# Kernel optimization log

Measured on AMD Instinct MI355X. Metric: run time of the kernel, lower is better.

Reference implementation:

```python
import jax, jax.numpy as jnp
import numpy as np

B, N, D = 32, 1024, 256
NHID = 512
NHID_HALF = NHID // 2
NCLASS = 2


def _xavier(key, shape):
    fan_in, fan_out = shape
    lim = float(np.sqrt(6.0 / (fan_in + fan_out)))
    return jax.random.uniform(key, shape, jnp.float32, -lim, lim)


def setup_inputs() -> dict:
    key = jax.random.key(0)
    ks = jax.random.split(key, 10)
    x = jax.random.normal(ks[0], (B, N, D), jnp.float32)
    adj = jax.random.uniform(ks[1], (B, N, N), jnp.float32)
    adj = adj / jnp.sum(adj, axis=-1, keepdims=True)  # row-normalized (mean aggregation)
    # GraphConv weights: shape (2*in_dim, out_dim) due to concat([x, agg(x)])
    W1 = _xavier(ks[2], (2 * D, NHID))
    b1 = jnp.zeros((NHID,), jnp.float32)
    W2 = _xavier(ks[3], (2 * NHID, NHID))
    b2 = jnp.zeros((NHID,), jnp.float32)
    W3 = _xavier(ks[4], (2 * NHID, NHID_HALF))
    b3 = jnp.zeros((NHID_HALF,), jnp.float32)
    W4 = _xavier(ks[5], (2 * NHID_HALF, NHID_HALF))
    b4 = jnp.zeros((NHID_HALF,), jnp.float32)
    # classifier: Linear(256,256) + PReLU(256) + Linear(256,2)
    cW1 = _xavier(ks[6], (NHID_HALF, NHID_HALF))
    cb1 = jnp.zeros((NHID_HALF,), jnp.float32)
    alpha = jnp.full((NHID_HALF,), 0.25, jnp.float32)
    cW2 = _xavier(ks[7], (NHID_HALF, NCLASS))
    cb2 = jnp.zeros((NCLASS,), jnp.float32)
    return {"x": x, "adj": adj, "W1": W1, "b1": b1, "W2": W2, "b2": b2,
            "W3": W3, "b3": b3, "W4": W4, "b4": b4,
            "cW1": cW1, "cb1": cb1, "alpha": alpha, "cW2": cW2, "cb2": cb2}


def _graphconv(x, adj, W, b):
    agg = jnp.einsum('bnm,bmd->bnd', adj, x)          # mean aggregation (adj row-normalized)
    cat = jnp.concatenate([x, agg], axis=-1)          # [B, N, 2*d]
    return jax.nn.relu(jnp.einsum('bnd,df->bnf', cat, W) + b)


def reference(x, adj, W1, b1, W2, b2, W3, b3, W4, b4, cW1, cb1, alpha, cW2, cb2):
    h = _graphconv(x, adj, W1, b1)
    h = _graphconv(h, adj, W2, b2)
    h = _graphconv(h, adj, W3, b3)
    h = _graphconv(h, adj, W4, b4)
    # classifier MLP with channel-wise PReLU
    h = jnp.einsum('bnd,df->bnf', h, cW1) + cb1
    h = jnp.where(h > 0, h, alpha * h)
    pred = jnp.einsum('bnd,df->bnf', h, cW2) + cb2
    return pred
```

## Files before the change

### kernel.cpp

```cpp
#include <hip/hip_runtime.h>

typedef short v8s __attribute__((ext_vector_type(8)));
typedef _Float16 v8h __attribute__((ext_vector_type(8)));
typedef float v4f __attribute__((ext_vector_type(4)));

#define BMT 128
#define BNT 128
#define BKT 32

__device__ __forceinline__ unsigned short f2bf(float f) {
    unsigned int u = __float_as_uint(f);
    u += 0x7fff + ((u >> 16) & 1);
    return (unsigned short)(u >> 16);
}
__device__ __forceinline__ unsigned short f2h(float f) {
    union { _Float16 h; unsigned short u; } c;
    c.h = (_Float16)f;
    return c.u;
}
__device__ __forceinline__ float h2f(unsigned short v) {
    union { unsigned short u; _Float16 h; } c;
    c.u = v;
    return (float)c.h;
}
__device__ __forceinline__ v8h as_h(v8s x) {
    union { v8s s; v8h h; } c;
    c.s = x;
    return c.h;
}

union U128 { unsigned short s[8]; uint4 v; };

__device__ __forceinline__ void gld16(const unsigned short* g, unsigned short* l) {
    __builtin_amdgcn_global_load_lds((const __attribute__((address_space(1))) void*)g,
                                     (__attribute__((address_space(3))) void*)l, 16, 0, 0);
}

__global__ __launch_bounds__(256) void split_f16(const float* __restrict__ x,
                                                 unsigned short* __restrict__ o, int n4) {
    int i = blockIdx.x * 256 + threadIdx.x;
    if (i < n4) {
        float4 f = ((const float4*)x)[i];
        float fv[4] = {f.x, f.y, f.z, f.w};
        ushort4 h;
        unsigned short* hp = (unsigned short*)&h;
#pragma unroll
        for (int j = 0; j < 4; ++j) hp[j] = f2h(fv[j]);
        ((ushort4*)o)[i] = h;
    }
}

__global__ __launch_bounds__(256) void split_hi(const float* __restrict__ x,
                                                unsigned short* __restrict__ oh, int n4) {
    int i = blockIdx.x * 256 + threadIdx.x;
    if (i < n4) {
        float4 f = ((const float4*)x)[i];
        float fv[4] = {f.x, f.y, f.z, f.w};
        ushort4 h;
        unsigned short* hp = (unsigned short*)&h;
#pragma unroll
        for (int j = 0; j < 4; ++j) hp[j] = f2bf(fv[j]);
        ((ushort4*)oh)[i] = h;
    }
}

__global__ __launch_bounds__(256) void tsplit16(const float* __restrict__ W,
                                                unsigned short* __restrict__ th, int R, int C) {
    int e = blockIdx.x * 256 + threadIdx.x;
    if (e < R * C) {
        int k = e / C, n = e - k * C;
        th[(size_t)n * R + k] = f2h(W[e]);
    }
}

__global__ __launch_bounds__(256) void transp_x(const float* __restrict__ src,
                                                unsigned short* __restrict__ th, int d) {
    __shared__ unsigned int lds[64 * 66];
    const int t = threadIdx.x;
    const int mt = blockIdx.x, ft = blockIdx.y, z = blockIdx.z;
    const int r = t >> 3, c8 = (t & 7) * 8;
#pragma unroll
    for (int half = 0; half < 2; ++half) {
        int rr = r + half * 32;
        size_t grow = (size_t)z * 1024 + mt * 64 + rr;
        const float* xs = src + grow * d + ft * 64 + c8;
        float4 f0 = *(const float4*)xs;
        float4 f1 = *(const float4*)(xs + 4);
        float fv[8] = {f0.x, f0.y, f0.z, f0.w, f1.x, f1.y, f1.z, f1.w};
#pragma unroll
        for (int j = 0; j < 8; ++j)
            lds[rr * 66 + c8 + j] = f2bf(fv[j]);
    }
    __syncthreads();
    const int f = t >> 3, m0 = (t & 7) * 8;
#pragma unroll
    for (int half = 0; half < 2; ++half) {
        int ff = f + half * 32;
        U128 uh;
#pragma unroll
        for (int j = 0; j < 8; ++j)
            uh.s[j] = (unsigned short)lds[(m0 + j) * 66 + ff];
        size_t orow = ((size_t)z * d + ft * 64 + ff) * 1024 + mt * 64 + m0;
        *(uint4*)(th + orow) = uh.v;
    }
}

template <int ACT, bool TWO, int AMODE, int DT, bool WRT>
__global__ __launch_bounds__(256) void gemm128(
    const void* a1, const unsigned short* __restrict__ a2,
    int K1, int K2,
    const unsigned short* __restrict__ b_, int ldb,
    const float* __restrict__ bias, const float* __restrict__ alpha,
    unsigned short* __restrict__ o_, int Nout,
    unsigned short* __restrict__ th,
    size_t aZ, size_t bZ, int cZRows,
    int nblk, int mBits)
{
    constexpr int LA = (AMODE == 0) ? 32 : 40;
    constexpr int LB = 32;
    __shared__ __align__(16) unsigned short Ash[BMT * LA];
    __shared__ __align__(16) unsigned short Bsh[BNT * LB];

    const int t = threadIdx.x;
    const int lane = t & 63, wave = t >> 6;
    const int wm = wave >> 1, wn = wave & 1;
    const int l15 = lane & 15, quad = lane >> 4;

    const int bx = blockIdx.x;
    const int low3 = bx & 7, rest = bx >> 3;
    const int nIdx = rest % nblk, g = rest / nblk;
    const int grp = g * 8 + low3;
    const int m0 = (grp & ((1 << mBits) - 1)) * BMT;
    const int zb = grp >> mBits;
    const int n0 = nIdx * BNT;

    const unsigned short* bhz = b_ + (size_t)zb * bZ;

    v4f acc[4][4] = {};

    const int nch = TWO ? 2 : 1;
    for (int ch = 0; ch < nch; ++ch) {
        const int K = (TWO && ch) ? K2 : K1;
        const int kr0 = (TWO && ch) ? K1 : 0;
        const unsigned short* ah = nullptr;
        const float* af = nullptr;
        if constexpr (AMODE == 0)
            ah = (ch ? a2 : (const unsigned short*)a1) + (size_t)zb * aZ;
        else
            af = (const float*)a1 + (size_t)zb * aZ;

        for (int kk = 0; kk < K; kk += BKT) {
            __syncthreads();
            if constexpr (AMODE == 0) {
#pragma unroll
                for (int i = 0; i < 2; ++i) {
                    int s = i * 256 + t;
                    int row = s >> 2;
                    int cg = (s & 3) ^ ((s >> 3) & 3);
                    size_t go = (size_t)(m0 + row) * K + kk + cg * 8;
                    int ls = (i * 256 + (t & ~63)) * 8;
                    gld16(ah + go, &Ash[ls]);
                }
            } else {
#pragma unroll
                for (int i = 0; i < 2; ++i) {
                    int cid = i * 256 + t;
                    int row = cid >> 2, c = cid & 3;
                    const float* src = af + (size_t)(m0 + row) * K + kk + c * 8;
                    float4 f0 = *(const float4*)src;
                    float4 f1 = *(const float4*)(src + 4);
                    float fv[8] = {f0.x, f0.y, f0.z, f0.w, f1.x, f1.y, f1.z, f1.w};
                    U128 uh;
#pragma unroll
                    for (int j = 0; j < 8; ++j) uh.s[j] = f2bf(fv[j]);
                    *(uint4*)&Ash[row * LA + c * 8] = uh.v;
                }
            }
#pragma unroll
            for (int i = 0; i < 2; ++i) {
                int s = i * 256 + t;
                int row = s >> 2;
                int cg = (s & 3) ^ ((s >> 3) & 3);
                size_t go = (size_t)(n0 + row) * ldb + kr0 + kk + cg * 8;
                int ls = (i * 256 + (t & ~63)) * 8;
                gld16(bhz + go, &Bsh[ls]);
            }
            __syncthreads();
            v8s ahf[4];
#pragma unroll
            for (int mi = 0; mi < 4; ++mi) {
                int row = wm * 64 + mi * 16 + l15;
                int off;
                if constexpr (AMODE == 0) off = row * LA + ((quad ^ ((row >> 1) & 3)) * 8);
                else                      off = row * LA + quad * 8;
                ahf[mi] = *(const v8s*)&Ash[off];
            }
#pragma unroll
            for (int ni = 0; ni < 4; ++ni) {
                int row = wn * 64 + ni * 16 + l15;
                int off = row * LB + ((quad ^ ((row >> 1) & 3)) * 8);
                v8s bhf = *(const v8s*)&Bsh[off];
#pragma unroll
                for (int mi = 0; mi < 4; ++mi) {
                    if constexpr (DT == 0)
                        acc[mi][ni] = __builtin_amdgcn_mfma_f32_16x16x32_bf16(ahf[mi], bhf, acc[mi][ni], 0, 0, 0);
                    else
                        acc[mi][ni] = __builtin_amdgcn_mfma_f32_16x16x32_f16(as_h(ahf[mi]), as_h(bhf), acc[mi][ni], 0, 0, 0);
                }
            }
        }
    }

    const size_t crow0 = (size_t)zb * cZRows + m0;
#pragma unroll
    for (int ni = 0; ni < 4; ++ni) {
        int n = n0 + wn * 64 + ni * 16 + l15;
        float bv = (ACT > 0) ? bias[n] : 0.f;
        float av = (ACT == 2) ? alpha[n] : 0.f;
#pragma unroll
        for (int mi = 0; mi < 4; ++mi) {
#pragma unroll
            for (int r = 0; r < 4; ++r) {
                int m = wm * 64 + mi * 16 + quad * 4 + r;
                float v = acc[mi][ni][r] + bv;
                if (ACT == 1) v = v > 0.f ? v : 0.f;
                if (ACT == 2) v = v > 0.f ? v : av * v;
                acc[mi][ni][r] = v;
                o_[(crow0 + m) * (size_t)Nout + n] = f2h(v);
            }
        }
    }

    if constexpr (WRT) {
        const int zbT = m0 >> 10;
        const int mloc0 = (m0 & 1023) + wm * 64;
#pragma unroll
        for (int ni = 0; ni < 4; ++ni) {
            int f = n0 + wn * 64 + ni * 16 + l15;
            size_t rowb = (((size_t)zbT * Nout + f) << 10) + mloc0;
#pragma unroll
            for (int mi = 0; mi < 4; ++mi) {
                ushort4 u;
                unsigned short* up = (unsigned short*)&u;
#pragma unroll
                for (int r = 0; r < 4; ++r) up[r] = f2bf(acc[mi][ni][r]);
                *(ushort4*)(th + rowb + mi * 16 + quad * 4) = u;
            }
        }
    }
}

template <int ACT, bool TWO, int DT, bool WRT, int BN2>
__global__ __launch_bounds__(512, 2) void gemm256(
    const unsigned short* __restrict__ a1, const unsigned short* __restrict__ a2,
    int K1, int K2,
    const unsigned short* __restrict__ b_, int ldb,
    const float* __restrict__ bias, const float* __restrict__ alpha,
    unsigned short* __restrict__ o_, int Nout,
    unsigned short* __restrict__ th,
    size_t aZ, size_t bZ, int cZRows,
    int nblk, int mBits)
{
    constexpr int ASLOT = 256 * 32;
    constexpr int BSLOT = BN2 * 32;
    constexpr int SLOT  = ASLOT + BSLOT;
    constexpr int LPT   = 2 + BN2 / 128;
    constexpr int WN    = BN2 / 64;
    constexpr int WM    = 8 / WN;
    constexpr int MREP  = 16 / WM;
    __shared__ __align__(16) unsigned short lds[4 * SLOT];

    const int t = threadIdx.x;
    const int lane = t & 63, wave = t >> 6;
    const int wm = wave / WN, wn = wave % WN;
    const int l15 = lane & 15, quad = lane >> 4;

    const int bx = blockIdx.x;
    const int low3 = bx & 7, rest = bx >> 3;
    const int nIdx = rest % nblk, g = rest / nblk;
    const int grp = g * 8 + low3;
    const int m0 = (grp & ((1 << mBits) - 1)) * 256;
    const int zb = grp >> mBits;
    const int n0 = nIdx * BN2;

    const unsigned short* A1 = a1 + (size_t)zb * aZ;
    const unsigned short* A2p = TWO ? (a2 + (size_t)zb * aZ) : nullptr;
    const unsigned short* B = b_ + (size_t)zb * bZ;

    const int NT1 = K1 >> 5;
    const int NTtot = NT1 + (TWO ? (K2 >> 5) : 0);

    auto stage = [&](int tt) {
        unsigned short* slot = &lds[(tt & 3) * SLOT];
        const unsigned short* abase;
        int astr;
        if constexpr (TWO) {
            if (tt >= NT1) { abase = A2p + ((size_t)(tt - NT1) << 5); astr = K2; }
            else           { abase = A1 + ((size_t)tt << 5); astr = K1; }
        } else {
            abase = A1 + ((size_t)tt << 5); astr = K1;
        }
#pragma unroll
        for (int i = 0; i < 2; ++i) {
            int s = i * 512 + t;
            int row = s >> 2;
            int cg = (s & 3) ^ ((s >> 3) & 3);
            gld16(abase + (size_t)(m0 + row) * astr + cg * 8,
                  &slot[(i * 512 + (t & ~63)) * 8]);
        }
        const unsigned short* bbase = B + ((size_t)tt << 5);
#pragma unroll
        for (int i = 0; i < BN2 / 128; ++i) {
            int s = i * 512 + t;
            int row = s >> 2;
            int cg = (s & 3) ^ ((s >> 3) & 3);
            gld16(bbase + (size_t)(n0 + row) * ldb + cg * 8,
                  &slot[ASLOT + (i * 512 + (t & ~63)) * 8]);
        }
    };

    auto rdfrags = [&](int tt, v8s (&AF)[MREP], v8s (&BF)[4]) {
        const unsigned short* slot = &lds[(tt & 3) * SLOT];
#pragma unroll
        for (int mi = 0; mi < MREP; ++mi) {
            int row = wm * (MREP * 16) + mi * 16 + l15;
            AF[mi] = *(const v8s*)&slot[row * 32 + ((quad ^ ((row >> 1) & 3)) * 8)];
        }
#pragma unroll
        for (int ni = 0; ni < 4; ++ni) {
            int row = wn * 64 + ni * 16 + l15;
            BF[ni] = *(const v8s*)&slot[ASLOT + row * 32 + ((quad ^ ((row >> 1) & 3)) * 8)];
        }
    };

    v4f acc[MREP][4] = {};

    auto mfma_c = [&](v8s (&AF)[MREP], v8s (&BF)[4]) {
        __builtin_amdgcn_s_setprio(1);
#pragma unroll
        for (int ni = 0; ni < 4; ++ni) {
#pragma unroll
            for (int mi = 0; mi < MREP; ++mi) {
                if constexpr (DT == 0)
                    acc[mi][ni] = __builtin_amdgcn_mfma_f32_16x16x32_bf16(AF[mi], BF[ni], acc[mi][ni], 0, 0, 0);
                else
                    acc[mi][ni] = __builtin_amdgcn_mfma_f32_16x16x32_f16(as_h(AF[mi]), as_h(BF[ni]), acc[mi][ni], 0, 0, 0);
            }
        }
        __builtin_amdgcn_s_setprio(0);
    };

    auto wait_lpt = [&]() {
        if constexpr (LPT == 4) asm volatile("s_waitcnt vmcnt(4)" ::: "memory");
        else                    asm volatile("s_waitcnt vmcnt(3)" ::: "memory");
    };

    v8s afA[MREP], bfA[4], afB[MREP], bfB[4];

    stage(0); stage(1); stage(2);
    wait_lpt();
    __builtin_amdgcn_s_barrier();
    asm volatile("" ::: "memory");
    rdfrags(0, afA, bfA);

    for (int tt = 0; tt < NTtot; tt += 2) {
        if (tt + 3 < NTtot) stage(tt + 3);
        if (tt + 1 < NTtot) rdfrags(tt + 1, afB, bfB);
        mfma_c(afA, bfA);
        if (tt + 2 < NTtot) {
            if (tt + 3 < NTtot) wait_lpt();
            else                asm volatile("s_waitcnt vmcnt(0)" ::: "memory");
            __builtin_amdgcn_s_barrier();
            asm volatile("" ::: "memory");
        }
        if (tt + 4 < NTtot) stage(tt + 4);
        if (tt + 2 < NTtot) rdfrags(tt + 2, afA, bfA);
        mfma_c(afB, bfB);
        if (tt + 3 < NTtot) {
            if (tt + 4 < NTtot) wait_lpt();
            else                asm volatile("s_waitcnt vmcnt(0)" ::: "memory");
            __builtin_amdgcn_s_barrier();
            asm volatile("" ::: "memory");
        }
    }

    const size_t crow0 = (size_t)zb * cZRows + m0;
#pragma unroll
    for (int ni = 0; ni < 4; ++ni) {
        int n = n0 + wn * 64 + ni * 16 + l15;
        float bv = (ACT > 0) ? bias[n] : 0.f;
        float av = (ACT == 2) ? alpha[n] : 0.f;
#pragma unroll
        for (int mi = 0; mi < MREP; ++mi) {
#pragma unroll
            for (int r = 0; r < 4; ++r) {
                int m = wm * (MREP * 16) + mi * 16 + quad * 4 + r;
                float v = acc[mi][ni][r] + bv;
                if (ACT == 1) v = v > 0.f ? v : 0.f;
                if (ACT == 2) v = v > 0.f ? v : av * v;
                acc[mi][ni][r] = v;
                o_[(crow0 + m) * (size_t)Nout + n] = f2h(v);
            }
        }
    }

    if constexpr (WRT) {
        const int zbT = m0 >> 10;
        const int mloc0 = (m0 & 1023) + wm * (MREP * 16);
#pragma unroll
        for (int ni = 0; ni < 4; ++ni) {
            int f = n0 + wn * 64 + ni * 16 + l15;
            size_t rowb = (((size_t)zbT * Nout + f) << 10) + mloc0;
#pragma unroll
            for (int mi = 0; mi < MREP; ++mi) {
                ushort4 u;
                unsigned short* up = (unsigned short*)&u;
#pragma unroll
                for (int r = 0; r < 4; ++r) up[r] = f2bf(acc[mi][ni][r]);
                *(ushort4*)(th + rowb + mi * 16 + quad * 4) = u;
            }
        }
    }
}

__global__ __launch_bounds__(256) void final_gemm(const unsigned short* __restrict__ hh,
                                                  const float* __restrict__ W,
                                                  const float* __restrict__ bias,
                                                  float* __restrict__ out) {
    const int t = threadIdx.x;
    const int m = blockIdx.x * 64 + (t >> 2);
    const int kq = (t & 3) * 64;
    const unsigned short* ph = hh + (size_t)m * 256 + kq;
    float a0 = 0.f, a1 = 0.f;
#pragma unroll
    for (int i = 0; i < 8; ++i) {
        uint4 vh = *(const uint4*)(ph + i * 8);
        const unsigned short* sh = (const unsigned short*)&vh;
#pragma unroll
        for (int j = 0; j < 8; ++j) {
            int k = kq + i * 8 + j;
            float h = h2f(sh[j]);
            a0 += h * W[k * 2];
            a1 += h * W[k * 2 + 1];
        }
    }
    a0 += __shfl_down(a0, 2); a0 += __shfl_down(a0, 1);
    a1 += __shfl_down(a1, 2); a1 += __shfl_down(a1, 1);
    if ((t & 3) == 0) {
        out[(size_t)m * 2] = a0 + bias[0];
        out[(size_t)m * 2 + 1] = a1 + bias[1];
    }
}

extern "C" void kernel_launch(void* const* d_in, const int* in_sizes, int n_in,
                              void* d_out, int out_size, void* d_ws, size_t ws_size,
                              hipStream_t stream) {
    const float* x   = (const float*)d_in[0];
    const float* adj = (const float*)d_in[1];
    const float* W1  = (const float*)d_in[2];
    const float* b1  = (const float*)d_in[3];
    const float* W2  = (const float*)d_in[4];
    const float* b2  = (const float*)d_in[5];
    const float* W3  = (const float*)d_in[6];
    const float* b3  = (const float*)d_in[7];
    const float* W4  = (const float*)d_in[8];
    const float* b4  = (const float*)d_in[9];
    const float* cW1 = (const float*)d_in[10];
    const float* cb1 = (const float*)d_in[11];
    const float* alp = (const float*)d_in[12];
    const float* cW2 = (const float*)d_in[13];
    const float* cb2 = (const float*)d_in[14];
    float* out = (float*)d_out;

    const size_t P   = 32768ull * 512;
    const size_t XP  = 32768ull * 256;
    const size_t WT_TOT = 1245184;
    const size_t ADJ = 32ull * 1024 * 1024;

    unsigned short* N1  = (unsigned short*)d_ws;
    unsigned short* N2  = N1 + P;
    unsigned short* N3  = N2 + P;
    unsigned short* Th  = N3 + P;
    unsigned short* X16 = Th + P;
    unsigned short* WT  = X16 + XP;
    unsigned short* SA  = WT + WT_TOT;

    const size_t o1 = 0, o2 = 262144, o3 = 786432, o4 = 1048576, o5 = 1179648;
    const bool preAdj = ws_size >= (4 * P + XP + WT_TOT + ADJ) * sizeof(unsigned short);

    dim3 blk(256);
    dim3 blk5(512);

    split_f16<<<8192, blk, 0, stream>>>(x, X16, (int)(XP / 4));
    tsplit16<<<1024, blk, 0, stream>>>(W1,  WT + o1, 512, 512);
    tsplit16<<<2048, blk, 0, stream>>>(W2,  WT + o2, 1024, 512);
    tsplit16<<<1024, blk, 0, stream>>>(W3,  WT + o3, 1024, 256);
    tsplit16<<<512,  blk, 0, stream>>>(W4,  WT + o4, 512, 256);
    tsplit16<<<256,  blk, 0, stream>>>(cW1, WT + o5, 256, 256);
    if (preAdj)
        split_hi<<<32768, blk, 0, stream>>>(adj, SA, (int)(ADJ / 4));

    transp_x<<<dim3(16, 4, 32), blk, 0, stream>>>(x, Th, 256);

    if (preAdj)
        gemm256<0, false, 0, false, 128><<<256, blk5, 0, stream>>>(
            SA, nullptr, 1024, 0, Th, 1024, nullptr, nullptr,
            N2, 256, nullptr, (size_t)1 << 20, 256ull * 1024, 1024, 2, 2);
    else
        gemm128<0, false, 1, 0, false><<<512, blk, 0, stream>>>(
            adj, nullptr, 1024, 0, Th, 1024, nullptr, nullptr,
            N2, 256, nullptr, (size_t)1 << 20, 256ull * 1024, 1024, 2, 3);

    gemm256<1, true, 1, true, 256><<<256, blk5, 0, stream>>>(
        X16, N2, 256, 256, WT + o1, 512, b1, nullptr,
        N3, 512, Th, 0, 0, 0, 2, 7);

    if (preAdj)
        gemm256<0, false, 0, false, 256><<<256, blk5, 0, stream>>>(
            SA, nullptr, 1024, 0, Th, 1024, nullptr, nullptr,
            N1, 512, nullptr, (size_t)1 << 20, 512ull * 1024, 1024, 2, 2);
    else
        gemm128<0, false, 1, 0, false><<<1024, blk, 0, stream>>>(
            adj, nullptr, 1024, 0, Th, 1024, nullptr, nullptr,
            N1, 512, nullptr, (size_t)1 << 20, 512ull * 1024, 1024, 4, 3);

    gemm256<1, true, 1, true, 256><<<256, blk5, 0, stream>>>(
        N3, N1, 512, 512, WT + o2, 1024, b2, nullptr,
        N2, 512, Th, 0, 0, 0, 2, 7);

    if (preAdj)
        gemm256<0, false, 0, false, 256><<<256, blk5, 0, stream>>>(
            SA, nullptr, 1024, 0, Th, 1024, nullptr, nullptr,
            N1, 512, nullptr, (size_t)1 << 20, 512ull * 1024, 1024, 2, 2);
    else
        gemm128<0, false, 1, 0, false><<<1024, blk, 0, stream>>>(
            adj, nullptr, 1024, 0, Th, 1024, nullptr, nullptr,
            N1, 512, nullptr, (size_t)1 << 20, 512ull * 1024, 1024, 4, 3);

    gemm256<1, true, 1, true, 128><<<256, blk5, 0, stream>>>(
        N2, N1, 512, 512, WT + o3, 1024, b3, nullptr,
        N3, 256, Th, 0, 0, 0, 2, 7);

    if (preAdj)
        gemm256<0, false, 0, false, 128><<<256, blk5, 0, stream>>>(
            SA, nullptr, 1024, 0, Th, 1024, nullptr, nullptr,
            N1, 256, nullptr, (size_t)1 << 20, 256ull * 1024, 1024, 2, 2);
    else
        gemm128<0, false, 1, 0, false><<<512, blk, 0, stream>>>(
            adj, nullptr, 1024, 0, Th, 1024, nullptr, nullptr,
            N1, 256, nullptr, (size_t)1 << 20, 256ull * 1024, 1024, 2, 3);

    gemm256<1, true, 1, false, 128><<<256, blk5, 0, stream>>>(
        N3, N1, 256, 256, WT + o4, 512, b4, nullptr,
        N2, 256, nullptr, 0, 0, 0, 2, 7);

    gemm256<2, false, 1, false, 128><<<256, blk5, 0, stream>>>(
        N2, nullptr, 256, 0, WT + o5, 256, cb1, alp,
        N3, 256, nullptr, 0, 0, 0, 2, 7);

    final_gemm<<<512, blk, 0, stream>>>(N3, cW2, cb2, out);
}
```

Baseline: 553.5 us.

## Interleave staged loads with MFMA phases, fuse x conversion, tile weight transposes

The gemm256 main loop now handles one K-tile per iteration. It is split into phases: each phase reads two A fragments, issues one portion of the next tile's global-to-LDS loads, and then runs its MFMAs. This is meant to spread memory traffic across the compute instead of issuing it all at once. The separate fp16 conversion of x is folded into the transpose kernel, which removes one full pass over x. The weight transpose kernels now use LDS tiles to get coalesced stores. The cost is an extra barrier per phase and the loss of the double-buffered fragment registers, which could expose LDS read latency.

```diff
diff --git a/kernel.cpp b/kernel.cpp
--- a/kernel.cpp
+++ b/kernel.cpp
@@ -34,20 +34,6 @@
 __device__ __forceinline__ void gld16(const unsigned short* g, unsigned short* l) {
     __builtin_amdgcn_global_load_lds((const __attribute__((address_space(1))) void*)g,
                                      (__attribute__((address_space(3))) void*)l, 16, 0, 0);
-}
-
-__global__ __launch_bounds__(256) void split_f16(const float* __restrict__ x,
-                                                 unsigned short* __restrict__ o, int n4) {
-    int i = blockIdx.x * 256 + threadIdx.x;
-    if (i < n4) {
-        float4 f = ((const float4*)x)[i];
-        float fv[4] = {f.x, f.y, f.z, f.w};
-        ushort4 h;
-        unsigned short* hp = (unsigned short*)&h;
-#pragma unroll
-        for (int j = 0; j < 4; ++j) hp[j] = f2h(fv[j]);
-        ((ushort4*)o)[i] = h;
-    }
 }
 
 __global__ __launch_bounds__(256) void split_hi(const float* __restrict__ x,
@@ -66,15 +52,32 @@
 
 __global__ __launch_bounds__(256) void tsplit16(const float* __restrict__ W,
                                                 unsigned short* __restrict__ th, int R, int C) {
-    int e = blockIdx.x * 256 + threadIdx.x;
-    if (e < R * C) {
-        int k = e / C, n = e - k * C;
-        th[(size_t)n * R + k] = f2h(W[e]);
-    }
-}
-
-__global__ __launch_bounds__(256) void transp_x(const float* __restrict__ src,
-                                                unsigned short* __restrict__ th, int d) {
+    __shared__ unsigned short lds[64][80];
+    const int t = threadIdx.x;
+    const int rt = blockIdx.x, ct = blockIdx.y;
+    const int r = t >> 2, c0 = (t & 3) * 16;
+    const float* src = W + (size_t)(rt * 64 + r) * C + ct * 64 + c0;
+#pragma unroll
+    for (int j = 0; j < 16; j += 4) {
+        float4 f = *(const float4*)(src + j);
+        lds[c0 + j + 0][r] = f2h(f.x);
+        lds[c0 + j + 1][r] = f2h(f.y);
+        lds[c0 + j + 2][r] = f2h(f.z);
+        lds[c0 + j + 3][r] = f2h(f.w);
+    }
+    __syncthreads();
+    const int c = t >> 2, r0 = (t & 3) * 16;
+    U128 u0, u1;
+#pragma unroll
+    for (int j = 0; j < 8; ++j) { u0.s[j] = lds[c][r0 + j]; u1.s[j] = lds[c][r0 + 8 + j]; }
+    unsigned short* dst = th + (size_t)(ct * 64 + c) * R + rt * 64 + r0;
+    *(uint4*)dst = u0.v;
+    *(uint4*)(dst + 8) = u1.v;
+}
+
+__global__ __launch_bounds__(256) void xprep(const float* __restrict__ src,
+                                             unsigned short* __restrict__ th,
+                                             unsigned short* __restrict__ x16, int d) {
     __shared__ unsigned int lds[64 * 66];
     const int t = threadIdx.x;
     const int mt = blockIdx.x, ft = blockIdx.y, z = blockIdx.z;
@@ -87,9 +90,13 @@
         float4 f0 = *(const float4*)xs;
         float4 f1 = *(const float4*)(xs + 4);
         float fv[8] = {f0.x, f0.y, f0.z, f0.w, f1.x, f1.y, f1.z, f1.w};
-#pragma unroll
-        for (int j = 0; j < 8; ++j)
+        U128 uh;
+#pragma unroll
+        for (int j = 0; j < 8; ++j) {
             lds[rr * 66 + c8 + j] = f2bf(fv[j]);
+            uh.s[j] = f2h(fv[j]);
+        }
+        *(uint4*)(x16 + grow * d + ft * 64 + c8) = uh.v;
     }
     __syncthreads();
     const int f = t >> 3, m0 = (t & 7) * 8;
@@ -268,6 +275,7 @@
     constexpr int WN    = BN2 / 64;
     constexpr int WM    = 8 / WN;
     constexpr int MREP  = 16 / WM;
+    constexpr int NPH   = MREP / 2;
     __shared__ __align__(16) unsigned short lds[4 * SLOT];
 
     const int t = threadIdx.x;
@@ -290,7 +298,7 @@
     const int NT1 = K1 >> 5;
     const int NTtot = NT1 + (TWO ? (K2 >> 5) : 0);
 
-    auto stage = [&](int tt) {
+    auto stage_part = [&](int tt, int p) {
         unsigned short* slot = &lds[(tt & 3) * SLOT];
         const unsigned short* abase;
         int astr;
@@ -300,54 +308,41 @@
         } else {
             abase = A1 + ((size_t)tt << 5); astr = K1;
         }
-#pragma unroll
-        for (int i = 0; i < 2; ++i) {
+        auto lda = [&](int i) {
             int s = i * 512 + t;
             int row = s >> 2;
             int cg = (s & 3) ^ ((s >> 3) & 3);
             gld16(abase + (size_t)(m0 + row) * astr + cg * 8,
                   &slot[(i * 512 + (t & ~63)) * 8]);
-        }
-        const unsigned short* bbase = B + ((size_t)tt << 5);
-#pragma unroll
-        for (int i = 0; i < BN2 / 128; ++i) {
+        };
+        auto ldb_ = [&](int i) {
+            const unsigned short* bbase = B + ((size_t)tt << 5);
             int s = i * 512 + t;
             int row = s >> 2;
             int cg = (s & 3) ^ ((s >> 3) & 3);
             gld16(bbase + (size_t)(n0 + row) * ldb + cg * 8,
                   &slot[ASLOT + (i * 512 + (t & ~63)) * 8]);
+        };
+        if constexpr (BN2 == 256) {
+            if (p < 2) lda(p); else ldb_(p - 2);
+        } else {
+            if (p == 0) { lda(0); lda(1); } else ldb_(0);
         }
     };
-
-    auto rdfrags = [&](int tt, v8s (&AF)[MREP], v8s (&BF)[4]) {
-        const unsigned short* slot = &lds[(tt & 3) * SLOT];
-#pragma unroll
-        for (int mi = 0; mi < MREP; ++mi) {
-            int row = wm * (MREP * 16) + mi * 16 + l15;
-            AF[mi] = *(const v8s*)&slot[row * 32 + ((quad ^ ((row >> 1) & 3)) * 8)];
-        }
-#pragma unroll
-        for (int ni = 0; ni < 4; ++ni) {
-            int row = wn * 64 + ni * 16 + l15;
-            BF[ni] = *(const v8s*)&slot[ASLOT + row * 32 + ((quad ^ ((row >> 1) & 3)) * 8)];
-        }
+    auto stage_all = [&](int tt) {
+#pragma unroll
+        for (int p = 0; p < NPH; ++p) stage_part(tt, p);
     };
 
     v4f acc[MREP][4] = {};
 
-    auto mfma_c = [&](v8s (&AF)[MREP], v8s (&BF)[4]) {
-        __builtin_amdgcn_s_setprio(1);
-#pragma unroll
-        for (int ni = 0; ni < 4; ++ni) {
-#pragma unroll
-            for (int mi = 0; mi < MREP; ++mi) {
-                if constexpr (DT == 0)
-                    acc[mi][ni] = __builtin_amdgcn_mfma_f32_16x16x32_bf16(AF[mi], BF[ni], acc[mi][ni], 0, 0, 0);
-                else
-                    acc[mi][ni] = __builtin_amdgcn_mfma_f32_16x16x32_f16(as_h(AF[mi]), as_h(BF[ni]), acc[mi][ni], 0, 0, 0);
-            }
-        }
-        __builtin_amdgcn_s_setprio(0);
+    auto rdA = [&](const unsigned short* slot, int mi) -> v8s {
+        int row = wm * (MREP * 16) + mi * 16 + l15;
+        return *(const v8s*)&slot[row * 32 + ((quad ^ ((row >> 1) & 3)) * 8)];
+    };
+    auto rdB = [&](const unsigned short* slot, int ni) -> v8s {
+        int row = wn * 64 + ni * 16 + l15;
+        return *(const v8s*)&slot[ASLOT + row * 32 + ((quad ^ ((row >> 1) & 3)) * 8)];
     };
 
     auto wait_lpt = [&]() {
@@ -355,29 +350,41 @@
         else                    asm volatile("s_waitcnt vmcnt(3)" ::: "memory");
     };
 
-    v8s afA[MREP], bfA[4], afB[MREP], bfB[4];
-
-    stage(0); stage(1); stage(2);
+    stage_all(0); stage_all(1); stage_all(2);
     wait_lpt();
     __builtin_amdgcn_s_barrier();
     asm volatile("" ::: "memory");
-    rdfrags(0, afA, bfA);
-
-    for (int tt = 0; tt < NTtot; tt += 2) {
-        if (tt + 3 < NTtot) stage(tt + 3);
-        if (tt + 1 < NTtot) rdfrags(tt + 1, afB, bfB);
-        mfma_c(afA, bfA);
+
+    for (int tt = 0; tt < NTtot; ++tt) {
+        const unsigned short* slot = &lds[(tt & 3) * SLOT];
+        const bool st = (tt + 3 < NTtot);
+        v8s bf[4];
+#pragma unroll
+        for (int q = 0; q < NPH; ++q) {
+            if (q == 0) {
+#pragma unroll
+                for (int ni = 0; ni < 4; ++ni) bf[ni] = rdB(slot, ni);
+            }
+            v8s a0 = rdA(slot, 2 * q);
+            v8s a1 = rdA(slot, 2 * q + 1);
+            if (st) stage_part(tt + 3, q);
+            __builtin_amdgcn_s_barrier();
+            asm volatile("" ::: "memory");
+            __builtin_amdgcn_s_setprio(1);
+#pragma unroll
+            for (int ni = 0; ni < 4; ++ni) {
+                if constexpr (DT == 0) {
+                    acc[2 * q][ni]     = __builtin_amdgcn_mfma_f32_16x16x32_bf16(a0, bf[ni], acc[2 * q][ni], 0, 0, 0);
+                    acc[2 * q + 1][ni] = __builtin_amdgcn_mfma_f32_16x16x32_bf16(a1, bf[ni], acc[2 * q + 1][ni], 0, 0, 0);
+                } else {
+                    acc[2 * q][ni]     = __builtin_amdgcn_mfma_f32_16x16x32_f16(as_h(a0), as_h(bf[ni]), acc[2 * q][ni], 0, 0, 0);
+                    acc[2 * q + 1][ni] = __builtin_amdgcn_mfma_f32_16x16x32_f16(as_h(a1), as_h(bf[ni]), acc[2 * q + 1][ni], 0, 0, 0);
+                }
+            }
+            __builtin_amdgcn_s_setprio(0);
+        }
         if (tt + 2 < NTtot) {
             if (tt + 3 < NTtot) wait_lpt();
-            else                asm volatile("s_waitcnt vmcnt(0)" ::: "memory");
-            __builtin_amdgcn_s_barrier();
-            asm volatile("" ::: "memory");
-        }
-        if (tt + 4 < NTtot) stage(tt + 4);
-        if (tt + 2 < NTtot) rdfrags(tt + 2, afA, bfA);
-        mfma_c(afB, bfB);
-        if (tt + 3 < NTtot) {
-            if (tt + 4 < NTtot) wait_lpt();
             else                asm volatile("s_waitcnt vmcnt(0)" ::: "memory");
             __builtin_amdgcn_s_barrier();
             asm volatile("" ::: "memory");
@@ -491,16 +498,15 @@
     dim3 blk(256);
     dim3 blk5(512);
 
-    split_f16<<<8192, blk, 0, stream>>>(x, X16, (int)(XP / 4));
-    tsplit16<<<1024, blk, 0, stream>>>(W1,  WT + o1, 512, 512);
-    tsplit16<<<2048, blk, 0, stream>>>(W2,  WT + o2, 1024, 512);
-    tsplit16<<<1024, blk, 0, stream>>>(W3,  WT + o3, 1024, 256);
-    tsplit16<<<512,  blk, 0, stream>>>(W4,  WT + o4, 512, 256);
-    tsplit16<<<256,  blk, 0, stream>>>(cW1, WT + o5, 256, 256);
+    tsplit16<<<dim3(8, 8),  blk, 0, stream>>>(W1,  WT + o1, 512, 512);
+    tsplit16<<<dim3(16, 8), blk, 0, stream>>>(W2,  WT + o2, 1024, 512);
+    tsplit16<<<dim3(16, 4), blk, 0, stream>>>(W3,  WT + o3, 1024, 256);
+    tsplit16<<<dim3(8, 4),  blk, 0, stream>>>(W4,  WT + o4, 512, 256);
+    tsplit16<<<dim3(4, 4),  blk, 0, stream>>>(cW1, WT + o5, 256, 256);
     if (preAdj)
         split_hi<<<32768, blk, 0, stream>>>(adj, SA, (int)(ADJ / 4));
 
-    transp_x<<<dim3(16, 4, 32), blk, 0, stream>>>(x, Th, 256);
+    xprep<<<dim3(16, 4, 32), blk, 0, stream>>>(x, Th, X16, 256);
 
     if (preAdj)
         gemm256<0, false, 0, false, 128><<<256, blk5, 0, stream>>>(
```

New measurement: 554.1 us. Within noise of the previous version (+0.1%).
